# Optimization experiments

Hardware: AMD Instinct MI355X
Metric: run time of the kernel (lower is better)

The kernel has to match this reference:

```python
import jax, jax.numpy as jnp
import numpy as np

IMG_H, IMG_W = 800.0, 1280.0
STRIDE = 16
SCALE = 1.0 / STRIDE
P, S = 14, 1              # pooler resolution, sampling ratio
NUM_CLASSES = 80
BBOX_W = (10.0, 10.0, 5.0, 5.0)
SCORE_TH, NMS_TH, MAX_DET, IOU_TH = 0.05, 0.5, 100, 0.5
SCALE_CLAMP = float(np.log(1000.0 / 16.0))


def _make_boxes(key, n_img, n_box):
    k1, k2, k3, k4 = jax.random.split(key, 4)
    x1 = jax.random.uniform(k1, (n_img, n_box)) * (IMG_W - 64.0)
    y1 = jax.random.uniform(k2, (n_img, n_box)) * (IMG_H - 64.0)
    w = jax.random.uniform(k3, (n_img, n_box)) * 300.0 + 16.0
    h = jax.random.uniform(k4, (n_img, n_box)) * 300.0 + 16.0
    x2 = jnp.minimum(x1 + w, IMG_W)
    y2 = jnp.minimum(y1 + h, IMG_H)
    return jnp.stack([x1, y1, x2, y2], axis=-1)


def setup_inputs() -> dict:
    key = jax.random.key(0)
    ks = jax.random.split(key, 6)
    features = jax.random.normal(ks[0], (2, 50, 80, 1024), dtype=jnp.float32)
    proposals = _make_boxes(ks[1], 2, 256)
    gt_boxes = _make_boxes(ks[2], 2, 64)
    gt_classes = jax.random.randint(ks[3], (2, 64), 0, NUM_CLASSES)
    W_cls = jax.random.normal(ks[4], (1024, NUM_CLASSES + 1), dtype=jnp.float32) * 0.01
    b_cls = jnp.zeros((NUM_CLASSES + 1,), jnp.float32)
    W_box = jax.random.normal(ks[5], (1024, 4), dtype=jnp.float32) * 0.01
    b_box = jnp.zeros((4,), jnp.float32)
    return {"features": features, "proposals": proposals, "gt_boxes": gt_boxes,
            "gt_classes": gt_classes, "W_cls": W_cls, "b_cls": b_cls,
            "W_box": W_box, "b_box": b_box}


def pairwise_iou(a, b):
    # a: [G,4], b: [R,4], boxes as (x1,y1,x2,y2) -> [G,R]
    area_a = (a[:, 2] - a[:, 0]) * (a[:, 3] - a[:, 1])
    area_b = (b[:, 2] - b[:, 0]) * (b[:, 3] - b[:, 1])
    lt = jnp.maximum(a[:, None, :2], b[None, :, :2])
    rb = jnp.minimum(a[:, None, 2:], b[None, :, 2:])
    wh = jnp.clip(rb - lt, 0.0)
    inter = wh[..., 0] * wh[..., 1]
    return inter / jnp.maximum(area_a[:, None] + area_b[None, :] - inter, 1e-9)


def roi_align_one(feat, boxes):
    # feat: [H,W,C], boxes: [R,4] in image coords -> pooled [R,P,P,C]
    H, W, C = feat.shape
    b = boxes * SCALE
    x1, y1, x2, y2 = b[:, 0], b[:, 1], b[:, 2], b[:, 3]
    off = (jnp.arange(S, dtype=feat.dtype) + 0.5) / S       # [S]
    grid = jnp.arange(P, dtype=feat.dtype)                   # [P]
    bh = ((y2 - y1) / P)[:, None, None]
    bw = ((x2 - x1) / P)[:, None, None]
    # aligned RoIAlign sample coords (half-pixel offset)
    gy = y1[:, None, None] + (grid[None, :, None] + off[None, None, :]) * bh - 0.5  # [R,P,S]
    gx = x1[:, None, None] + (grid[None, :, None] + off[None, None, :]) * bw - 0.5
    gy = jnp.clip(gy, 0.0, H - 1.0)
    gx = jnp.clip(gx, 0.0, W - 1.0)
    y0 = jnp.floor(gy); x0 = jnp.floor(gx)
    y0i = y0.astype(jnp.int32); x0i = x0.astype(jnp.int32)
    y1i = jnp.minimum(y0i + 1, H - 1); x1i = jnp.minimum(x0i + 1, W - 1)
    ly = gy - y0; lx = gx - x0

    def g(yi, xi):  # cross-product gather -> [R,P,S,P,S,C]
        return feat[yi[:, :, :, None, None], xi[:, None, None, :, :]]

    wy0 = (1.0 - ly)[:, :, :, None, None, None]; wy1 = ly[:, :, :, None, None, None]
    wx0 = (1.0 - lx)[:, None, None, :, :, None]; wx1 = lx[:, None, None, :, :, None]
    val = wy0 * (wx0 * g(y0i, x0i) + wx1 * g(y0i, x1i)) \
        + wy1 * (wx0 * g(y1i, x0i) + wx1 * g(y1i, x1i))
    return val.mean(axis=(2, 4))  # average sampling points per bin -> [R,P,P,C]


def decode_boxes(deltas, boxes):
    wx, wy, ww, wh = BBOX_W
    widths = boxes[..., 2] - boxes[..., 0]
    heights = boxes[..., 3] - boxes[..., 1]
    ctr_x = boxes[..., 0] + 0.5 * widths
    ctr_y = boxes[..., 1] + 0.5 * heights
    dx = deltas[..., 0] / wx
    dy = deltas[..., 1] / wy
    dw = jnp.minimum(deltas[..., 2] / ww, SCALE_CLAMP)
    dh = jnp.minimum(deltas[..., 3] / wh, SCALE_CLAMP)
    pcx = dx * widths + ctr_x
    pcy = dy * heights + ctr_y
    pw = jnp.exp(dw) * widths
    ph = jnp.exp(dh) * heights
    out = jnp.stack([pcx - 0.5 * pw, pcy - 0.5 * ph, pcx + 0.5 * pw, pcy + 0.5 * ph], axis=-1)
    lim = jnp.array([IMG_W, IMG_H, IMG_W, IMG_H], out.dtype)
    return jnp.clip(out, 0.0, lim)


def nms_keep(boxes, scores):
    # greedy class-agnostic NMS, fixed-size keep mask [R]
    R = scores.shape[0]
    order = jnp.argsort(-scores)
    sb = boxes[order]
    iou = pairwise_iou(sb, sb)
    idx = jnp.arange(R)

    def body(i, keep):
        suppressed = jnp.any((idx < i) & keep & (iou[:, i] > NMS_TH))
        return keep.at[i].set(jnp.logical_not(suppressed))

    keep_sorted = jax.lax.fori_loop(0, R, body, jnp.ones((R,), bool))
    return jnp.zeros((R,), bool).at[order].set(keep_sorted)


def reference(features, proposals, gt_boxes, gt_classes, W_cls, b_cls, W_box, b_box):
    N, R = proposals.shape[:2]
    # --- proposal <-> gt matching (training-side labeling) ---
    iou_m = jax.vmap(pairwise_iou)(gt_boxes, proposals)          # [N,G,R]
    matched_vals = iou_m.max(axis=1)
    matched_idxs = iou_m.argmax(axis=1)                          # [N,R]
    match_labels = (matched_vals >= IOU_TH).astype(jnp.int32)    # [N,R] fg=1/bg=0
    # --- RoIAlign pooling on the single C4 feature map ---
    pooled = jax.vmap(roi_align_one)(features, proposals)        # [N,R,P,P,C]
    feat_vec = pooled.mean(axis=(2, 3))                          # res5 surrogate global avg -> [N,R,C]
    # --- box predictor ---
    scores_all = jax.nn.softmax(feat_vec @ W_cls + b_cls, axis=-1)
    fg_scores = scores_all[..., :NUM_CLASSES].max(axis=-1)       # drop background column
    deltas = feat_vec @ W_box + b_box
    boxes = decode_boxes(deltas, proposals)                      # [N,R,4]
    # --- score threshold + NMS + top-k ---
    keep = jax.vmap(nms_keep)(boxes, fg_scores) & (fg_scores > SCORE_TH)
    masked = jnp.where(keep, fg_scores, -jnp.inf)
    rank = jnp.argsort(jnp.argsort(-masked, axis=-1), axis=-1)
    keep = keep & (rank < MAX_DET)
    det = jnp.concatenate([boxes, fg_scores[..., None], keep.astype(boxes.dtype)[..., None]], axis=-1)
    return det, matched_idxs, match_labels
```

## Files before the change

### kernel.cpp

```cpp
#include <hip/hip_runtime.h>
#include <math.h>

#define N_IMG 2
#define R_PROP 256
#define G_GT 64
#define C_CH 1024
#define FH 50
#define FW 80
#define P_POOL 14
#define NCLS 80
#define IMG_W_F 1280.0f
#define IMG_H_F 800.0f
#define SCALE_F 0.0625f
#define SCORE_TH_F 0.05f
#define NMS_TH_F 0.5f
#define IOU_TH_F 0.5f
#define MAX_DET_I 100
#define SCALE_CLAMP_F 4.135166556742356f

__global__ __launch_bounds__(512) void sort_kernel(
    const float* __restrict__ proposals,
    int* __restrict__ perm) {
  const int t = threadIdx.x;
  const int n = t >> 8;
  __shared__ float cy[N_IMG * R_PROP];
  const float* pb = proposals + (size_t)t * 4;
  cy[t] = pb[1] + pb[3];
  __syncthreads();
  float my = cy[t];
  int rk = 0;
  const int base = n * R_PROP;
#pragma unroll 8
  for (int j = base; j < base + R_PROP; ++j) {
    float cj = cy[j];
    rk += (cj < my) || (cj == my && j < t);
  }
  perm[base + rk] = t & 255;
}

__global__ __launch_bounds__(256) void match_kernel(
    const float* __restrict__ proposals,
    const float* __restrict__ gt_boxes,
    float* __restrict__ out_idx,
    float* __restrict__ out_lbl) {
  int t = blockIdx.x * blockDim.x + threadIdx.x;
  if (t >= N_IMG * R_PROP) return;
  int n = t / R_PROP;
  const float* pb = proposals + (size_t)t * 4;
  float bx1 = pb[0], by1 = pb[1], bx2 = pb[2], by2 = pb[3];
  float area_b = (bx2 - bx1) * (by2 - by1);
  float best = -1.0f;
  int bidx = 0;
  const float* gt = gt_boxes + (size_t)n * G_GT * 4;
#pragma unroll 4
  for (int g = 0; g < G_GT; ++g) {
    float gx1 = gt[g * 4 + 0], gy1 = gt[g * 4 + 1];
    float gx2 = gt[g * 4 + 2], gy2 = gt[g * 4 + 3];
    float area_a = (gx2 - gx1) * (gy2 - gy1);
    float ix1 = fmaxf(gx1, bx1), iy1 = fmaxf(gy1, by1);
    float ix2 = fminf(gx2, bx2), iy2 = fminf(gy2, by2);
    float iw = fmaxf(ix2 - ix1, 0.0f), ih = fmaxf(iy2 - iy1, 0.0f);
    float inter = iw * ih;
    float iou = inter / fmaxf(area_a + area_b - inter, 1e-9f);
    if (iou > best) { best = iou; bidx = g; }
  }
  out_idx[t] = (float)bidx;
  out_lbl[t] = (best >= IOU_TH_F) ? 1.0f : 0.0f;
}

__global__ __launch_bounds__(1024) void roi_kernel(
    const float* __restrict__ features,
    const float* __restrict__ proposals,
    const int* __restrict__ perm,
    float* __restrict__ feat_vec) {
  const int b = blockIdx.x;
  const int xcd = b & 7;
  const int slot = b >> 3;
  const int n = xcd >> 2;
  const int band = xcd & 3;
  const int blk = n * R_PROP + perm[n * R_PROP + band * 64 + slot];

  const float* feat = features + (size_t)n * (FH * FW * C_CH);
  const int t = threadIdx.x;
  const int c4 = t & 255;
  const int g = t >> 8;

  __shared__ float s_Wy[FH];
  __shared__ float s_Wx[FW];
  __shared__ int s_b[4];
  __shared__ float4 s_red[3][256];

  if (t < FH) s_Wy[t] = 0.0f;
  if (t >= 128 && t < 128 + FW) s_Wx[t - 128] = 0.0f;
  __syncthreads();

  if (t < 2 * P_POOL) {
    const float* pb = proposals + (size_t)blk * 4;
    bool isY = t < P_POOL;
    int i = isY ? t : t - P_POOL;
    float lo = isY ? pb[1] : pb[0];
    float hi = isY ? pb[3] : pb[2];
    float limit = isY ? (float)(FH - 1) : (float)(FW - 1);
    float b1 = lo * SCALE_F, b2 = hi * SCALE_F;
    float bs = (b2 - b1) * (1.0f / P_POOL);
    float gg = b1 + ((float)i + 0.5f) * bs - 0.5f;
    gg = fminf(fmaxf(gg, 0.0f), limit);
    float fl = floorf(gg);
    int i0 = (int)fl;
    int i1 = min(i0 + 1, (int)limit);
    float l = gg - fl;
    if (isY) {
      atomicAdd(&s_Wy[i0], 1.0f - l);
      atomicAdd(&s_Wy[i1], l);
      if (i == 0) s_b[0] = i0;
      if (i == P_POOL - 1) s_b[1] = i1;
    } else {
      atomicAdd(&s_Wx[i0], 1.0f - l);
      atomicAdd(&s_Wx[i1], l);
      if (i == 0) s_b[2] = i0;
      if (i == P_POOL - 1) s_b[3] = i1;
    }
  }
  __syncthreads();

  const int ylo = s_b[0], yhi = s_b[1], xlo = s_b[2], xhi = s_b[3];
  float4 acc = make_float4(0.f, 0.f, 0.f, 0.f);
  for (int y = ylo + g; y <= yhi; y += 4) {
    float wy = s_Wy[y];
    const float4* row = (const float4*)(feat + (size_t)y * (FW * C_CH)) + c4;
#pragma unroll 8
    for (int x = xlo; x <= xhi; ++x) {
      float w = wy * s_Wx[x];
      float4 f = row[x * (C_CH / 4)];
      acc.x += w * f.x;
      acc.y += w * f.y;
      acc.z += w * f.z;
      acc.w += w * f.w;
    }
  }
  if (g > 0) s_red[g - 1][c4] = acc;
  __syncthreads();

  if (g == 0) {
    float4 a0 = s_red[0][c4];
    float4 a1 = s_red[1][c4];
    float4 a2 = s_red[2][c4];
    const float inv = 1.0f / (float)(P_POOL * P_POOL);
    float4 r;
    r.x = (acc.x + a0.x + a1.x + a2.x) * inv;
    r.y = (acc.y + a0.y + a1.y + a2.y) * inv;
    r.z = (acc.z + a0.z + a1.z + a2.z) * inv;
    r.w = (acc.w + a0.w + a1.w + a2.w) * inv;
    ((float4*)(feat_vec + (size_t)blk * C_CH))[c4] = r;
  }
}

__global__ __launch_bounds__(1024) void heads_kernel(
    const float* __restrict__ feat_vec,
    const float* __restrict__ proposals,
    const float* __restrict__ W_cls,
    const float* __restrict__ b_cls,
    const float* __restrict__ W_box,
    const float* __restrict__ b_box,
    float* __restrict__ boxes_dec,
    float* __restrict__ scores) {
  const int blk = blockIdx.x;
  const int u = threadIdx.x;
  __shared__ float sf[C_CH];
  __shared__ float s_part[12][85];
  __shared__ float sl[85];
  __shared__ float s_red[8];

  sf[u] = feat_vec[(size_t)blk * C_CH + u];
  __syncthreads();

  const int kq = u / 85;
  const int j = u - kq * 85;
  if (kq < 12) {
    float acc = 0.0f;
    if (j < 81) {
      const float* __restrict__ w = W_cls + j;
#pragma unroll 8
      for (int k = kq; k < C_CH; k += 12) acc += sf[k] * w[k * 81];
    } else {
      const float* __restrict__ w = W_box + (j - 81);
#pragma unroll 8
      for (int k = kq; k < C_CH; k += 12) acc += sf[k] * w[k * 4];
    }
    s_part[kq][j] = acc;
  }
  __syncthreads();

  if (u < 85) {
    float acc = (u < 81) ? b_cls[u] : b_box[u - 81];
#pragma unroll
    for (int p = 0; p < 12; ++p) acc += s_part[p][u];
    sl[u] = acc;
  }
  __syncthreads();

  if (u < 128) {
    float xm = (u < 81) ? sl[u] : -INFINITY;
    float xf = (u < NCLS) ? sl[u] : -INFINITY;
#pragma unroll
    for (int off = 32; off; off >>= 1) {
      xm = fmaxf(xm, __shfl_down(xm, off, 64));
      xf = fmaxf(xf, __shfl_down(xf, off, 64));
    }
    if ((u & 63) == 0) { s_red[u >> 6] = xm; s_red[2 + (u >> 6)] = xf; }
  }
  __syncthreads();
  const float m = fmaxf(s_red[0], s_red[1]);
  if (u < 128) {
    float xs = (u < 81) ? expf(sl[u] - m) : 0.0f;
#pragma unroll
    for (int off = 32; off; off >>= 1) xs += __shfl_down(xs, off, 64);
    if ((u & 63) == 0) s_red[4 + (u >> 6)] = xs;
  }
  __syncthreads();

  if (u == 0) {
    float sum = s_red[4] + s_red[5];
    float fgm = fmaxf(s_red[2], s_red[3]);
    scores[blk] = expf(fgm - m) / sum;

    const float* pb = proposals + (size_t)blk * 4;
    float w = pb[2] - pb[0], h = pb[3] - pb[1];
    float cx = pb[0] + 0.5f * w, cy = pb[1] + 0.5f * h;
    float dx = sl[81] * 0.1f;
    float dy = sl[82] * 0.1f;
    float dw = fminf(sl[83] * 0.2f, SCALE_CLAMP_F);
    float dh = fminf(sl[84] * 0.2f, SCALE_CLAMP_F);
    float pcx = dx * w + cx, pcy = dy * h + cy;
    float pw = expf(dw) * w, ph = expf(dh) * h;
    float ox1 = fminf(fmaxf(pcx - 0.5f * pw, 0.0f), IMG_W_F);
    float oy1 = fminf(fmaxf(pcy - 0.5f * ph, 0.0f), IMG_H_F);
    float ox2 = fminf(fmaxf(pcx + 0.5f * pw, 0.0f), IMG_W_F);
    float oy2 = fminf(fmaxf(pcy + 0.5f * ph, 0.0f), IMG_H_F);
    float* bd = boxes_dec + (size_t)blk * 4;
    bd[0] = ox1; bd[1] = oy1; bd[2] = ox2; bd[3] = oy2;
  }
}

__global__ __launch_bounds__(1024) void nms_kernel(
    const float* __restrict__ boxes_dec,
    const float* __restrict__ scores,
    float* __restrict__ det) {
  const int n = blockIdx.x;
  const int u = threadIdx.x;
  const int i = u & 255;
  const int q = u >> 8;
  const int j40 = q * 16;

  __shared__ __align__(16) float ss[R_PROP];
  __shared__ float4 sbs[R_PROP];
  __shared__ int s_part[4 * R_PROP];
  __shared__ int s_rank[R_PROP];
  __shared__ __align__(16) unsigned long long s_mask[R_PROP * 4];
  __shared__ unsigned long long s_keep[4];
  __shared__ __align__(16) float sm[R_PROP];

  float4 myb;
  float mys;
  if (q == 0) {
    myb = ((const float4*)boxes_dec)[n * R_PROP + i];
    mys = scores[n * R_PROP + i];
    ss[i] = mys;
  }
  __syncthreads();

  {
    float s = ss[i];
    int cnt = 0;
#pragma unroll
    for (int j4 = j40; j4 < j40 + 16; ++j4) {
      float4 v = ((const float4*)ss)[j4];
      int jb = j4 * 4;
      cnt += (v.x > s) || (v.x == s && jb + 0 < i);
      cnt += (v.y > s) || (v.y == s && jb + 1 < i);
      cnt += (v.z > s) || (v.z == s && jb + 2 < i);
      cnt += (v.w > s) || (v.w == s && jb + 3 < i);
    }
    s_part[q * R_PROP + i] = cnt;
  }
  __syncthreads();
  if (q == 0) {
    int rk = s_part[i] + s_part[R_PROP + i] + s_part[2 * R_PROP + i] +
             s_part[3 * R_PROP + i];
    s_rank[i] = rk;
    sbs[rk] = myb;
  }
  __syncthreads();

  {
    float4 bi = sbs[i];
    float area_i = (bi.z - bi.x) * (bi.w - bi.y);
    unsigned long long m = 0;
    const int j0 = q * 64;
#pragma unroll 8
    for (int jj = 0; jj < 64; ++jj) {
      float4 bj = sbs[j0 + jj];
      float area_j = (bj.z - bj.x) * (bj.w - bj.y);
      float ix1 = fmaxf(bi.x, bj.x), iy1 = fmaxf(bi.y, bj.y);
      float ix2 = fminf(bi.z, bj.z), iy2 = fminf(bi.w, bj.w);
      float iw = fmaxf(ix2 - ix1, 0.0f), ih = fmaxf(iy2 - iy1, 0.0f);
      float inter = iw * ih;
      float iou = inter / fmaxf(area_i + area_j - inter, 1e-9f);
      m |= (iou > NMS_TH_F) ? (1ull << jj) : 0ull;
    }
    s_mask[i * 4 + q] = m;
  }
  __syncthreads();

  if (u == 0) {
    unsigned long long K0 = ~0ull, K1 = ~0ull, K2 = ~0ull, K3 = ~0ull;
#pragma unroll 16
    for (int b = 1; b < 64; ++b) {
      unsigned long long m0 = s_mask[(size_t)b * 4 + 0];
      unsigned long long sup = m0 & K0 & ((1ull << b) - 1ull);
      K0 = sup ? (K0 & ~(1ull << b)) : K0;
    }
#pragma unroll 16
    for (int b = 0; b < 64; ++b) {
      const unsigned long long* mi = &s_mask[(size_t)(64 + b) * 4];
      unsigned long long m0 = mi[0], m1 = mi[1];
      unsigned long long sup = (m0 & K0) | (m1 & K1 & ((1ull << b) - 1ull));
      K1 = sup ? (K1 & ~(1ull << b)) : K1;
    }
#pragma unroll 16
    for (int b = 0; b < 64; ++b) {
      const unsigned long long* mi = &s_mask[(size_t)(128 + b) * 4];
      unsigned long long m0 = mi[0], m1 = mi[1], m2 = mi[2];
      unsigned long long sup =
          (m0 & K0) | (m1 & K1) | (m2 & K2 & ((1ull << b) - 1ull));
      K2 = sup ? (K2 & ~(1ull << b)) : K2;
    }
#pragma unroll 16
    for (int b = 0; b < 64; ++b) {
      const unsigned long long* mi = &s_mask[(size_t)(192 + b) * 4];
      unsigned long long m0 = mi[0], m1 = mi[1], m2 = mi[2], m3 = mi[3];
      unsigned long long sup = (m0 & K0) | (m1 & K1) | (m2 & K2) |
                               (m3 & K3 & ((1ull << b) - 1ull));
      K3 = sup ? (K3 & ~(1ull << b)) : K3;
    }
    s_keep[0] = K0; s_keep[1] = K1; s_keep[2] = K2; s_keep[3] = K3;
  }
  __syncthreads();

  bool kept = false;
  if (q == 0) {
    int rk = s_rank[i];
    kept = ((s_keep[rk >> 6] >> (rk & 63)) & 1ull) && (mys > SCORE_TH_F);
    sm[i] = kept ? mys : -INFINITY;
  }
  __syncthreads();

  {
    float mym = sm[i];
    int cnt = 0;
#pragma unroll
    for (int j4 = j40; j4 < j40 + 16; ++j4) {
      float4 v = ((const float4*)sm)[j4];
      int jb = j4 * 4;
      cnt += (v.x > mym) || (v.x == mym && jb + 0 < i);
      cnt += (v.y > mym) || (v.y == mym && jb + 1 < i);
      cnt += (v.z > mym) || (v.z == mym && jb + 2 < i);
      cnt += (v.w > mym) || (v.w == mym && jb + 3 < i);
    }
    s_part[q * R_PROP + i] = cnt;
  }
  __syncthreads();

  if (q == 0) {
    int rk2 = s_part[i] + s_part[R_PROP + i] + s_part[2 * R_PROP + i] +
              s_part[3 * R_PROP + i];
    kept = kept && (rk2 < MAX_DET_I);
    float* dr = det + ((size_t)n * R_PROP + i) * 6;
    dr[0] = myb.x; dr[1] = myb.y; dr[2] = myb.z; dr[3] = myb.w;
    dr[4] = mys;
    dr[5] = kept ? 1.0f : 0.0f;
  }
}

extern "C" void kernel_launch(void* const* d_in, const int* in_sizes, int n_in,
                              void* d_out, int out_size, void* d_ws, size_t ws_size,
                              hipStream_t stream) {
  const float* features  = (const float*)d_in[0];
  const float* proposals = (const float*)d_in[1];
  const float* gt_boxes  = (const float*)d_in[2];
  const float* W_cls = (const float*)d_in[4];
  const float* b_cls = (const float*)d_in[5];
  const float* W_box = (const float*)d_in[6];
  const float* b_box = (const float*)d_in[7];

  float* out = (float*)d_out;
  float* out_det = out;
  float* out_idx = out + N_IMG * R_PROP * 6;
  float* out_lbl = out_idx + N_IMG * R_PROP;

  float* feat_vec  = (float*)d_ws;
  float* boxes_dec = feat_vec + (size_t)N_IMG * R_PROP * C_CH;
  float* scores    = boxes_dec + (size_t)N_IMG * R_PROP * 4;
  int*   perm      = (int*)(scores + N_IMG * R_PROP);

  sort_kernel<<<1, 512, 0, stream>>>(proposals, perm);
  match_kernel<<<2, 256, 0, stream>>>(proposals, gt_boxes, out_idx, out_lbl);
  roi_kernel<<<N_IMG * R_PROP, 1024, 0, stream>>>(features, proposals, perm,
                                                  feat_vec);
  heads_kernel<<<N_IMG * R_PROP, 1024, 0, stream>>>(feat_vec, proposals, W_cls,
                                                    b_cls, W_box, b_box,
                                                    boxes_dec, scores);
  nms_kernel<<<N_IMG, 1024, 0, stream>>>(boxes_dec, scores, out_det);
}
```

Before: 171.5 us.

## Fuse RoI pooling with box heads and merge sort with GT matching

Merges the proposal sort and GT matching into one single-block prep kernel. It also fuses the RoIAlign pooling kernel with the classification/box-head kernel, so the pooled feature vector stays in shared memory and is never written to or read back from global workspace. This drops two kernel launches and a 2 MB global round trip. In exchange the fused block uses more shared memory and runs the head GEMV tail inside the memory-bound pooling blocks, which may lower overlap.

```diff
diff --git a/kernel.cpp b/kernel.cpp
--- a/kernel.cpp
+++ b/kernel.cpp
@@ -18,61 +18,64 @@
 #define MAX_DET_I 100
 #define SCALE_CLAMP_F 4.135166556742356f
 
-__global__ __launch_bounds__(512) void sort_kernel(
+__global__ __launch_bounds__(512) void prep_kernel(
     const float* __restrict__ proposals,
-    int* __restrict__ perm) {
+    const float* __restrict__ gt_boxes,
+    int* __restrict__ perm,
+    float* __restrict__ out_idx,
+    float* __restrict__ out_lbl) {
   const int t = threadIdx.x;
   const int n = t >> 8;
   __shared__ float cy[N_IMG * R_PROP];
   const float* pb = proposals + (size_t)t * 4;
-  cy[t] = pb[1] + pb[3];
-  __syncthreads();
-  float my = cy[t];
-  int rk = 0;
-  const int base = n * R_PROP;
-#pragma unroll 8
-  for (int j = base; j < base + R_PROP; ++j) {
-    float cj = cy[j];
-    rk += (cj < my) || (cj == my && j < t);
-  }
-  perm[base + rk] = t & 255;
+  float bx1 = pb[0], by1 = pb[1], bx2 = pb[2], by2 = pb[3];
+  cy[t] = by1 + by2;
+  __syncthreads();
+
+  {
+    float my = cy[t];
+    int rk = 0;
+    const int base = n * R_PROP;
+#pragma unroll 8
+    for (int j = base; j < base + R_PROP; ++j) {
+      float cj = cy[j];
+      rk += (cj < my) || (cj == my && j < t);
+    }
+    perm[base + rk] = t & 255;
+  }
+
+  {
+    float area_b = (bx2 - bx1) * (by2 - by1);
+    float best = -1.0f;
+    int bidx = 0;
+    const float* gt = gt_boxes + (size_t)n * G_GT * 4;
+#pragma unroll 4
+    for (int g = 0; g < G_GT; ++g) {
+      float gx1 = gt[g * 4 + 0], gy1 = gt[g * 4 + 1];
+      float gx2 = gt[g * 4 + 2], gy2 = gt[g * 4 + 3];
+      float area_a = (gx2 - gx1) * (gy2 - gy1);
+      float ix1 = fmaxf(gx1, bx1), iy1 = fmaxf(gy1, by1);
+      float ix2 = fminf(gx2, bx2), iy2 = fminf(gy2, by2);
+      float iw = fmaxf(ix2 - ix1, 0.0f), ih = fmaxf(iy2 - iy1, 0.0f);
+      float inter = iw * ih;
+      float iou = inter / fmaxf(area_a + area_b - inter, 1e-9f);
+      if (iou > best) { best = iou; bidx = g; }
+    }
+    out_idx[t] = (float)bidx;
+    out_lbl[t] = (best >= IOU_TH_F) ? 1.0f : 0.0f;
+  }
 }
 
-__global__ __launch_bounds__(256) void match_kernel(
-    const float* __restrict__ proposals,
-    const float* __restrict__ gt_boxes,
-    float* __restrict__ out_idx,
-    float* __restrict__ out_lbl) {
-  int t = blockIdx.x * blockDim.x + threadIdx.x;
-  if (t >= N_IMG * R_PROP) return;
-  int n = t / R_PROP;
-  const float* pb = proposals + (size_t)t * 4;
-  float bx1 = pb[0], by1 = pb[1], bx2 = pb[2], by2 = pb[3];
-  float area_b = (bx2 - bx1) * (by2 - by1);
-  float best = -1.0f;
-  int bidx = 0;
-  const float* gt = gt_boxes + (size_t)n * G_GT * 4;
-#pragma unroll 4
-  for (int g = 0; g < G_GT; ++g) {
-    float gx1 = gt[g * 4 + 0], gy1 = gt[g * 4 + 1];
-    float gx2 = gt[g * 4 + 2], gy2 = gt[g * 4 + 3];
-    float area_a = (gx2 - gx1) * (gy2 - gy1);
-    float ix1 = fmaxf(gx1, bx1), iy1 = fmaxf(gy1, by1);
-    float ix2 = fminf(gx2, bx2), iy2 = fminf(gy2, by2);
-    float iw = fmaxf(ix2 - ix1, 0.0f), ih = fmaxf(iy2 - iy1, 0.0f);
-    float inter = iw * ih;
-    float iou = inter / fmaxf(area_a + area_b - inter, 1e-9f);
-    if (iou > best) { best = iou; bidx = g; }
-  }
-  out_idx[t] = (float)bidx;
-  out_lbl[t] = (best >= IOU_TH_F) ? 1.0f : 0.0f;
-}
-
-__global__ __launch_bounds__(1024) void roi_kernel(
+__global__ __launch_bounds__(1024) void roihead_kernel(
     const float* __restrict__ features,
     const float* __restrict__ proposals,
     const int* __restrict__ perm,
-    float* __restrict__ feat_vec) {
+    const float* __restrict__ W_cls,
+    const float* __restrict__ b_cls,
+    const float* __restrict__ W_box,
+    const float* __restrict__ b_box,
+    float* __restrict__ boxes_dec,
+    float* __restrict__ scores) {
   const int b = blockIdx.x;
   const int xcd = b & 7;
   const int slot = b >> 3;
@@ -89,6 +92,10 @@
   __shared__ float s_Wx[FW];
   __shared__ int s_b[4];
   __shared__ float4 s_red[3][256];
+  __shared__ __align__(16) float sf[C_CH];
+  __shared__ float s_part[12][85];
+  __shared__ float sl[85];
+  __shared__ float s_r2[8];
 
   if (t < FH) s_Wy[t] = 0.0f;
   if (t >= 128 && t < 128 + FW) s_Wx[t - 128] = 0.0f;
@@ -123,59 +130,41 @@
   }
   __syncthreads();
 
-  const int ylo = s_b[0], yhi = s_b[1], xlo = s_b[2], xhi = s_b[3];
-  float4 acc = make_float4(0.f, 0.f, 0.f, 0.f);
-  for (int y = ylo + g; y <= yhi; y += 4) {
-    float wy = s_Wy[y];
-    const float4* row = (const float4*)(feat + (size_t)y * (FW * C_CH)) + c4;
-#pragma unroll 8
-    for (int x = xlo; x <= xhi; ++x) {
-      float w = wy * s_Wx[x];
-      float4 f = row[x * (C_CH / 4)];
-      acc.x += w * f.x;
-      acc.y += w * f.y;
-      acc.z += w * f.z;
-      acc.w += w * f.w;
-    }
-  }
-  if (g > 0) s_red[g - 1][c4] = acc;
-  __syncthreads();
-
-  if (g == 0) {
-    float4 a0 = s_red[0][c4];
-    float4 a1 = s_red[1][c4];
-    float4 a2 = s_red[2][c4];
-    const float inv = 1.0f / (float)(P_POOL * P_POOL);
-    float4 r;
-    r.x = (acc.x + a0.x + a1.x + a2.x) * inv;
-    r.y = (acc.y + a0.y + a1.y + a2.y) * inv;
-    r.z = (acc.z + a0.z + a1.z + a2.z) * inv;
-    r.w = (acc.w + a0.w + a1.w + a2.w) * inv;
-    ((float4*)(feat_vec + (size_t)blk * C_CH))[c4] = r;
-  }
-}
-
-__global__ __launch_bounds__(1024) void heads_kernel(
-    const float* __restrict__ feat_vec,
-    const float* __restrict__ proposals,
-    const float* __restrict__ W_cls,
-    const float* __restrict__ b_cls,
-    const float* __restrict__ W_box,
-    const float* __restrict__ b_box,
-    float* __restrict__ boxes_dec,
-    float* __restrict__ scores) {
-  const int blk = blockIdx.x;
-  const int u = threadIdx.x;
-  __shared__ float sf[C_CH];
-  __shared__ float s_part[12][85];
-  __shared__ float sl[85];
-  __shared__ float s_red[8];
-
-  sf[u] = feat_vec[(size_t)blk * C_CH + u];
-  __syncthreads();
-
-  const int kq = u / 85;
-  const int j = u - kq * 85;
+  {
+    const int ylo = s_b[0], yhi = s_b[1], xlo = s_b[2], xhi = s_b[3];
+    float4 acc = make_float4(0.f, 0.f, 0.f, 0.f);
+    for (int y = ylo + g; y <= yhi; y += 4) {
+      float wy = s_Wy[y];
+      const float4* row = (const float4*)(feat + (size_t)y * (FW * C_CH)) + c4;
+#pragma unroll 8
+      for (int x = xlo; x <= xhi; ++x) {
+        float w = wy * s_Wx[x];
+        float4 f = row[x * (C_CH / 4)];
+        acc.x += w * f.x;
+        acc.y += w * f.y;
+        acc.z += w * f.z;
+        acc.w += w * f.w;
+      }
+    }
+    if (g > 0) s_red[g - 1][c4] = acc;
+    __syncthreads();
+    if (g == 0) {
+      float4 a0 = s_red[0][c4];
+      float4 a1 = s_red[1][c4];
+      float4 a2 = s_red[2][c4];
+      const float inv = 1.0f / (float)(P_POOL * P_POOL);
+      float4 r;
+      r.x = (acc.x + a0.x + a1.x + a2.x) * inv;
+      r.y = (acc.y + a0.y + a1.y + a2.y) * inv;
+      r.z = (acc.z + a0.z + a1.z + a2.z) * inv;
+      r.w = (acc.w + a0.w + a1.w + a2.w) * inv;
+      ((float4*)sf)[c4] = r;
+    }
+    __syncthreads();
+  }
+
+  const int kq = t / 85;
+  const int j = t - kq * 85;
   if (kq < 12) {
     float acc = 0.0f;
     if (j < 81) {
@@ -191,37 +180,37 @@
   }
   __syncthreads();
 
-  if (u < 85) {
-    float acc = (u < 81) ? b_cls[u] : b_box[u - 81];
-#pragma unroll
-    for (int p = 0; p < 12; ++p) acc += s_part[p][u];
-    sl[u] = acc;
-  }
-  __syncthreads();
-
-  if (u < 128) {
-    float xm = (u < 81) ? sl[u] : -INFINITY;
-    float xf = (u < NCLS) ? sl[u] : -INFINITY;
+  if (t < 85) {
+    float acc = (t < 81) ? b_cls[t] : b_box[t - 81];
+#pragma unroll
+    for (int p = 0; p < 12; ++p) acc += s_part[p][t];
+    sl[t] = acc;
+  }
+  __syncthreads();
+
+  if (t < 128) {
+    float xm = (t < 81) ? sl[t] : -INFINITY;
+    float xf = (t < NCLS) ? sl[t] : -INFINITY;
 #pragma unroll
     for (int off = 32; off; off >>= 1) {
       xm = fmaxf(xm, __shfl_down(xm, off, 64));
       xf = fmaxf(xf, __shfl_down(xf, off, 64));
     }
-    if ((u & 63) == 0) { s_red[u >> 6] = xm; s_red[2 + (u >> 6)] = xf; }
-  }
-  __syncthreads();
-  const float m = fmaxf(s_red[0], s_red[1]);
-  if (u < 128) {
-    float xs = (u < 81) ? expf(sl[u] - m) : 0.0f;
+    if ((t & 63) == 0) { s_r2[t >> 6] = xm; s_r2[2 + (t >> 6)] = xf; }
+  }
+  __syncthreads();
+  const float m = fmaxf(s_r2[0], s_r2[1]);
+  if (t < 128) {
+    float xs = (t < 81) ? expf(sl[t] - m) : 0.0f;
 #pragma unroll
     for (int off = 32; off; off >>= 1) xs += __shfl_down(xs, off, 64);
-    if ((u & 63) == 0) s_red[4 + (u >> 6)] = xs;
-  }
-  __syncthreads();
-
-  if (u == 0) {
-    float sum = s_red[4] + s_red[5];
-    float fgm = fmaxf(s_red[2], s_red[3]);
+    if ((t & 63) == 0) s_r2[4 + (t >> 6)] = xs;
+  }
+  __syncthreads();
+
+  if (t == 0) {
+    float sum = s_r2[4] + s_r2[5];
+    float fgm = fmaxf(s_r2[2], s_r2[3]);
     scores[blk] = expf(fgm - m) / sum;
 
     const float* pb = proposals + (size_t)blk * 4;
@@ -398,17 +387,12 @@
   float* out_idx = out + N_IMG * R_PROP * 6;
   float* out_lbl = out_idx + N_IMG * R_PROP;
 
-  float* feat_vec  = (float*)d_ws;
-  float* boxes_dec = feat_vec + (size_t)N_IMG * R_PROP * C_CH;
+  float* boxes_dec = (float*)d_ws;
   float* scores    = boxes_dec + (size_t)N_IMG * R_PROP * 4;
   int*   perm      = (int*)(scores + N_IMG * R_PROP);
 
-  sort_kernel<<<1, 512, 0, stream>>>(proposals, perm);
-  match_kernel<<<2, 256, 0, stream>>>(proposals, gt_boxes, out_idx, out_lbl);
-  roi_kernel<<<N_IMG * R_PROP, 1024, 0, stream>>>(features, proposals, perm,
-                                                  feat_vec);
-  heads_kernel<<<N_IMG * R_PROP, 1024, 0, stream>>>(feat_vec, proposals, W_cls,
-                                                    b_cls, W_box, b_box,
-                                                    boxes_dec, scores);
+  prep_kernel<<<1, 512, 0, stream>>>(proposals, gt_boxes, perm, out_idx, out_lbl);
+  roihead_kernel<<<N_IMG * R_PROP, 1024, 0, stream>>>(
+      features, proposals, perm, W_cls, b_cls, W_box, b_box, boxes_dec, scores);
   nms_kernel<<<N_IMG, 1024, 0, stream>>>(boxes_dec, scores, out_det);
 }
```

Measured after the change: 167.8 us. -2.1%, faster.
